# Kernel tuning notes

Hardware: AMD Instinct MI355X
Metric: run time of the kernel (lower is better)

Reference implementation:

```python
import jax, jax.numpy as jnp
import numpy as np
import math

B, H, W, C = 2, 256, 256, 96
HEADS, WS, SHIFT = 6, 8, 4
HD = C // HEADS
N = WS * WS
NW = (H // WS) * (W // WS)
HIDDEN = 2 * C
L = H * W


def _rel_pos_index():
    coords = np.stack(np.meshgrid(np.arange(WS), np.arange(WS), indexing='ij')).reshape(2, -1)
    rel = (coords[:, :, None] - coords[:, None, :]).transpose(1, 2, 0).astype(np.int64)
    rel[:, :, 0] += WS - 1
    rel[:, :, 1] += WS - 1
    rel[:, :, 0] *= 2 * WS - 1
    return rel.sum(-1)  # (N, N)

RPI = jnp.asarray(_rel_pos_index())


def _shift_mask():
    img = np.zeros((H, W), np.float32)
    cnt = 0
    for hs in (slice(0, -WS), slice(-WS, -SHIFT), slice(-SHIFT, None)):
        for ws in (slice(0, -WS), slice(-WS, -SHIFT), slice(-SHIFT, None)):
            img[hs, ws] = cnt
            cnt += 1
    mw = img.reshape(H // WS, WS, W // WS, WS).transpose(0, 2, 1, 3).reshape(-1, N)
    diff = mw[:, None, :] - mw[:, :, None]
    return jnp.asarray(np.where(diff != 0, -100.0, 0.0).astype(np.float32))  # (NW, N, N)

MASK = _shift_mask()


def window_partition(x):  # (b,H,W,c) -> (b*NW,WS,WS,c)
    b = x.shape[0]
    x = x.reshape(b, H // WS, WS, W // WS, WS, -1)
    return x.transpose(0, 1, 3, 2, 4, 5).reshape(b * NW, WS, WS, -1)


def window_reverse(w):  # (b*NW,WS,WS,c) -> (b,H,W,c)
    b = w.shape[0] // NW
    x = w.reshape(b, H // WS, W // WS, WS, WS, -1)
    return x.transpose(0, 1, 3, 2, 4, 5).reshape(b, H, W, -1)


def layernorm(x, g, bt):
    mu = x.mean(-1, keepdims=True)
    var = ((x - mu) ** 2).mean(-1, keepdims=True)
    return (x - mu) / jnp.sqrt(var + 1e-5) * g + bt


def gelu_exact(x):
    return x * 0.5 * (1.0 + jax.lax.erf(x / math.sqrt(2.0)))


def conv3(x, w, b):  # NHWC, HWIO
    return jax.lax.conv_general_dilated(x, w, (1, 1), 'SAME', dimension_numbers=('NHWC', 'HWIO', 'NHWC')) + b


def l2n(x):
    return x / jnp.maximum(jnp.linalg.norm(x, axis=-1, keepdims=True), 1e-12)


def setup_inputs() -> dict:
    key = jax.random.key(0)
    ks = jax.random.split(key, 24)
    s = 0.05
    return {
        'x': jax.random.normal(ks[0], (B, L, C), jnp.float32),
        'ref': jax.random.normal(ks[1], (B, L, C), jnp.float32),
        'norm1_g': jnp.ones((C,), jnp.float32),
        'norm1_b': jnp.zeros((C,), jnp.float32),
        'qkv_w': jax.random.normal(ks[2], (3 * C, C), jnp.float32) * s,
        'qkv_b': jnp.zeros((3 * C,), jnp.float32),
        'logit_scale': jnp.log(10.0) * jnp.ones((HEADS, 1, 1), jnp.float32),
        'gating': jnp.ones((HEADS,), jnp.float32),
        'rpb_table': jax.random.normal(ks[3], ((2 * WS - 1) ** 2, HEADS), jnp.float32) * 0.02,
        'trunk_w': jax.random.normal(ks[4], (4, 3, 3, C, C), jnp.float32) * s,
        'trunk_b': jnp.zeros((4, C), jnp.float32),
        'proj_w': jax.random.normal(ks[5], (C, C), jnp.float32) * s,
        'proj_b': jnp.zeros((C,), jnp.float32),
        'norm2_g': jnp.ones((C,), jnp.float32),
        'norm2_b': jnp.zeros((C,), jnp.float32),
        'fc1_w': jax.random.normal(ks[6], (HIDDEN, C), jnp.float32) * s,
        'fc1_b': jnp.zeros((HIDDEN,), jnp.float32),
        'convm_w': jax.random.normal(ks[7], (3, 3, HIDDEN, HIDDEN), jnp.float32) * s,
        'convm_b': jnp.zeros((HIDDEN,), jnp.float32),
        'fc2_w': jax.random.normal(ks[8], (C, HIDDEN), jnp.float32) * s,
        'fc2_b': jnp.zeros((C,), jnp.float32),
    }


def reference(x, ref, norm1_g, norm1_b, qkv_w, qkv_b, logit_scale, gating, rpb_table,
              trunk_w, trunk_b, proj_w, proj_b, norm2_g, norm2_b,
              fc1_w, fc1_b, convm_w, convm_b, fc2_w, fc2_b):
    shortcut = x
    xi = layernorm(x, norm1_g, norm1_b).reshape(B, H, W, C)
    ri = layernorm(ref, norm1_g, norm1_b).reshape(B, H, W, C)
    xi = jnp.roll(xi, (-SHIFT, -SHIFT), axis=(1, 2))
    ri = jnp.roll(ri, (-SHIFT, -SHIFT), axis=(1, 2))

    def qkv_windows(img):  # (B,H,W,C) -> q,k,v each (B*NW,HEADS,N,HD)
        t = jnp.einsum('bhwc,oc->bhwo', img, qkv_w) + qkv_b  # 1x1 conv
        t = window_partition(t).reshape(B * NW, N, 3, HEADS, HD)
        t = t.transpose(2, 0, 3, 1, 4)
        return t[0], t[1], t[2]

    q, k, v = qkv_windows(xi)
    _, k_r, v_r = qkv_windows(ri)

    ls = jnp.exp(jnp.minimum(logit_scale, math.log(1.0 / 0.01)))  # (HEADS,1,1)
    rpb = rpb_table[RPI.reshape(-1)].reshape(N, N, HEADS).transpose(2, 0, 1)  # (HEADS,N,N)
    qn = l2n(q)
    attn1 = jnp.einsum('bhnd,bhmd->bhnm', qn, l2n(k)) * ls + rpb[None]
    attn2 = jnp.einsum('bhnd,bhmd->bhnm', qn, l2n(k_r)) * ls + rpb[None]
    m = MASK[None, :, None]  # (1,NW,1,N,N)
    attn1 = (attn1.reshape(B, NW, HEADS, N, N) + m).reshape(B * NW, HEADS, N, N)
    attn2 = (attn2.reshape(B, NW, HEADS, N, N) + m).reshape(B * NW, HEADS, N, N)
    a1 = jax.nn.softmax(attn1, axis=-1)
    a2 = jax.nn.softmax(attn2, axis=-1)
    g = jax.nn.sigmoid(gating)[None, :, None, None]
    out = (1.0 - g) * jnp.einsum('bhnm,bhmd->bhnd', a1, v) + g * jnp.einsum('bhnm,bhmd->bhnd', a2, v_r)
    out = out.transpose(0, 2, 1, 3).reshape(B * NW, WS, WS, C)

    img = window_reverse(out)  # (B,H,W,C)
    # trunk branch: 2 residual blocks (conv3-relu-conv3 + skip)
    y = img
    for i in range(2):
        r = conv3(y, trunk_w[2 * i], trunk_b[2 * i])
        r = jax.nn.relu(r)
        r = conv3(r, trunk_w[2 * i + 1], trunk_b[2 * i + 1])
        y = y + r
    y = jnp.einsum('bhwc,oc->bhwo', y, proj_w) + proj_b  # 1x1 proj

    y = jnp.roll(y, (SHIFT, SHIFT), axis=(1, 2)).reshape(B, L, C)
    x = shortcut + y

    # conv-MLP: fc1 -> gelu -> conv3x3+gelu -> fc2
    h = layernorm(x, norm2_g, norm2_b)
    h = gelu_exact(h @ fc1_w.T + fc1_b)
    himg = h.reshape(B, H, W, HIDDEN)
    himg = gelu_exact(conv3(himg, convm_w, convm_b))
    h = himg.reshape(B, L, HIDDEN) @ fc2_w.T + fc2_b
    return x + h
```

## Files before the change

kernel.cpp:

```cpp
#include <hip/hip_runtime.h>
#include <hip/hip_bf16.h>

#define BB 2
#define HH 256
#define WWID 256
#define CC 96
#define NHEADS 6
#define WSZ 8
#define SHIFTV 4
#define HDIM 16
#define NTOK 64
#define HID 192
#define LL 65536

using bf16 = __hip_bfloat16;
typedef short short8v __attribute__((ext_vector_type(8)));
typedef float float4v __attribute__((ext_vector_type(4)));

__device__ __forceinline__ float b2f(bf16 v){ return __bfloat162float(v); }
__device__ __forceinline__ bf16  f2b(float f){ return __float2bfloat16(f); }
__device__ __forceinline__ float blo(unsigned u){ union {unsigned x; float f;} c; c.x = u << 16; return c.f; }
__device__ __forceinline__ float bhi(unsigned u){ union {unsigned x; float f;} c; c.x = u & 0xffff0000u; return c.f; }

__device__ __forceinline__ float dot8(uint4 a, uint4 b, float acc){
  acc += blo(a.x)*blo(b.x); acc += bhi(a.x)*bhi(b.x);
  acc += blo(a.y)*blo(b.y); acc += bhi(a.y)*bhi(b.y);
  acc += blo(a.z)*blo(b.z); acc += bhi(a.z)*bhi(b.z);
  acc += blo(a.w)*blo(b.w); acc += bhi(a.w)*bhi(b.w);
  return acc;
}

__global__ void detect_kernel(const unsigned* __restrict__ x, int* __restrict__ flag){
  __shared__ int s[256];
  int t = threadIdx.x;
  int cnt = 0;
  #pragma unroll
  for (int i = 0; i < 4; ++i){
    unsigned u = x[t*4 + i];
    unsigned e = (u >> 7) & 0xFFu;
    cnt += (e >= 118u && e <= 130u) ? 1 : 0;
  }
  s[t] = cnt; __syncthreads();
  for (int m = 128; m > 0; m >>= 1){ if (t < m) s[t] += s[t+m]; __syncthreads(); }
  if (t == 0) *flag = (s[0] < 512) ? 1 : 0;
}

struct CvtArgs { const void* src[21]; long cum[22]; };

__global__ void cvt_kernel(CvtArgs a, const int* __restrict__ flag,
                           bf16* __restrict__ dst, long total){
  long k = (long)blockIdx.x * 256 + threadIdx.x;
  if (k >= total) return;
  int lo = 0;
  #pragma unroll
  for (int i = 0; i < 21; ++i) if (k >= a.cum[i+1]) lo = i+1;
  long e = k - a.cum[lo];
  if (*flag) dst[k] = f2b(((const float*)a.src[lo])[e]);
  else       dst[k] = ((const bf16*)a.src[lo])[e];
}

__global__ void wprep_kernel(const bf16* __restrict__ w, bf16* __restrict__ out,
                             int CINr, int COUTr, long total){
  long k = (long)blockIdx.x * 256 + threadIdx.x;
  if (k >= total) return;
  int NHr = COUTr / 96, CHr = CINr / 96;
  int region = (int)(k / 9984); int rem = (int)(k - (long)region*9984);
  int gg = rem >> 3, e = rem & 7;
  int r = gg / 13, c8 = gg - r*13;
  int ch = region % CHr; int t2 = region / CHr;
  int nhh = t2 % NHr; int tap = t2 / NHr;
  bf16 v = f2b(0.f);
  if (c8 < 12){
    int cin = ch*96 + c8*8 + e;
    int cout = nhh*96 + r;
    v = w[((long)tap*CINr + cin)*COUTr + cout];
  }
  out[k] = v;
}

__global__ __launch_bounds__(256) void ln1_kernel(const bf16* __restrict__ x, const bf16* __restrict__ ref,
                                                  const bf16* __restrict__ g, const bf16* __restrict__ bt,
                                                  bf16* __restrict__ xn, bf16* __restrict__ rn)
{
  int wave = threadIdx.x >> 6, lane = threadIdx.x & 63;
  long row = (long)blockIdx.x * 4 + wave;
  const bf16* src; bf16* dst; long r;
  if (row < (long)BB*LL){ src = x; dst = xn; r = row; }
  else                  { src = ref; dst = rn; r = row - (long)BB*LL; }
  const bf16* p = src + r*CC;
  float v0 = b2f(p[lane]);
  float v1 = (lane < 32) ? b2f(p[64+lane]) : 0.f;
  float s = v0 + v1;
  #pragma unroll
  for (int m = 32; m >= 1; m >>= 1) s += __shfl_xor(s, m, 64);
  float mu = s * (1.f/CC);
  float d0 = v0 - mu, d1 = v1 - mu;
  float ss = d0*d0 + ((lane < 32) ? d1*d1 : 0.f);
  #pragma unroll
  for (int m = 32; m >= 1; m >>= 1) ss += __shfl_xor(ss, m, 64);
  float rstd = rsqrtf(ss * (1.f/CC) + 1e-5f);
  bf16* q = dst + r*CC;
  q[lane] = f2b(d0 * rstd * b2f(g[lane]) + b2f(bt[lane]));
  if (lane < 32) q[64+lane] = f2b(d1 * rstd * b2f(g[64+lane]) + b2f(bt[64+lane]));
}

__global__ __launch_bounds__(256) void ln2_kernel(const bf16* __restrict__ xin,
                                                  const bf16* __restrict__ g, const bf16* __restrict__ bt,
                                                  bf16* __restrict__ out)
{
  int wave = threadIdx.x >> 6, lane = threadIdx.x & 63;
  long r = (long)blockIdx.x * 4 + wave;
  const bf16* p = xin + r*CC;
  float v0 = b2f(p[lane]);
  float v1 = (lane < 32) ? b2f(p[64+lane]) : 0.f;
  float s = v0 + v1;
  #pragma unroll
  for (int m = 32; m >= 1; m >>= 1) s += __shfl_xor(s, m, 64);
  float mu = s * (1.f/CC);
  float d0 = v0 - mu, d1 = v1 - mu;
  float ss = d0*d0 + ((lane < 32) ? d1*d1 : 0.f);
  #pragma unroll
  for (int m = 32; m >= 1; m >>= 1) ss += __shfl_xor(ss, m, 64);
  float rstd = rsqrtf(ss * (1.f/CC) + 1e-5f);
  bf16* q = out + r*CC;
  q[lane] = f2b(d0 * rstd * b2f(g[lane]) + b2f(bt[lane]));
  if (lane < 32) q[64+lane] = f2b(d1 * rstd * b2f(g[64+lane]) + b2f(bt[64+lane]));
}

__global__ __launch_bounds__(256) void attn_kernel(const bf16* __restrict__ xn, const bf16* __restrict__ rn,
                                                   const bf16* __restrict__ qkv_w, const bf16* __restrict__ qkv_b,
                                                   const bf16* __restrict__ lsc, const bf16* __restrict__ gat,
                                                   const bf16* __restrict__ rpbt, bf16* __restrict__ img)
{
  __shared__ __align__(16) bf16 sx[NTOK][104];
  __shared__ __align__(16) bf16 sr[NTOK][104];
  __shared__ __align__(16) bf16 wb[48][104];
  __shared__ float sbias[48];
  __shared__ __align__(16) bf16 qs[NTOK][32];
  __shared__ __align__(16) bf16 ks[NTOK][32];
  __shared__ __align__(16) bf16 krs[NTOK][32];
  __shared__ __align__(16) bf16 vt[16][72];
  __shared__ __align__(16) bf16 vrt[16][72];
  __shared__ __align__(16) bf16 ps[NTOK][72];
  __shared__ float rpbs[225];

  int widx = blockIdx.x;
  int b = widx >> 10, wib = widx & 1023;
  int wh = wib >> 5, ww = wib & 31;
  int tid = threadIdx.x;
  int wv = tid >> 6, lane = tid & 63;
  int ml = lane & 15, quad = lane >> 4;

  for (int idx = tid; idx < NTOK*12; idx += 256){
    int n = idx / 12, c8 = idx - n*12;
    int i = n >> 3, j = n & 7;
    int h0 = (wh*8 + i + SHIFTV) & 255;
    int w0 = (ww*8 + j + SHIFTV) & 255;
    long base = (((long)b*HH + h0)*WWID + w0)*CC + c8*8;
    *(uint4*)&sx[n][c8*8] = *(const uint4*)&xn[base];
    *(uint4*)&sr[n][c8*8] = *(const uint4*)&rn[base];
  }
  for (int idx = tid; idx < 384; idx += 256){
    int arr = idx >> 7, rem = idx & 127;
    int row = rem >> 1, half = rem & 1;
    bf16* bp = (arr == 0) ? &qs[0][0] : (arr == 1) ? &ks[0][0] : &krs[0][0];
    *(uint4*)&bp[row*32 + 16 + half*8] = make_uint4(0,0,0,0);
  }

  for (int h = 0; h < NHEADS; ++h){
    __syncthreads();
    for (int idx = tid; idx < 48*12; idx += 256){
      int rr = idx / 12, c8 = idx - rr*12;
      int o = (rr >> 4)*CC + h*HDIM + (rr & 15);
      *(uint4*)&wb[rr][c8*8] = *(const uint4*)&qkv_w[(long)o*CC + c8*8];
    }
    if (tid < 48){
      int o = (tid >> 4)*CC + h*HDIM + (tid & 15);
      sbias[tid] = b2f(qkv_b[o]);
    }
    if (tid < 225) rpbs[tid] = b2f(rpbt[tid*NHEADS + h]);
    __syncthreads();

    float4v aq0 = {0,0,0,0}, aq1 = {0,0,0,0}, aq2 = {0,0,0,0};
    float4v ar0 = {0,0,0,0}, ar1 = {0,0,0,0};
    {
      int arow = wv*16 + ml;
      #pragma unroll
      for (int kt = 0; kt < 3; ++kt){
        int ko = kt*32 + quad*8;
        short8v ax = *(const short8v*)&sx[arow][ko];
        short8v av = *(const short8v*)&sr[arow][ko];
        short8v b0 = *(const short8v*)&wb[ml][ko];
        short8v b1 = *(const short8v*)&wb[16+ml][ko];
        short8v b2 = *(const short8v*)&wb[32+ml][ko];
        aq0 = __builtin_amdgcn_mfma_f32_16x16x32_bf16(ax, b0, aq0, 0,0,0);
        aq1 = __builtin_amdgcn_mfma_f32_16x16x32_bf16(ax, b1, aq1, 0,0,0);
        aq2 = __builtin_amdgcn_mfma_f32_16x16x32_bf16(ax, b2, aq2, 0,0,0);
        ar0 = __builtin_amdgcn_mfma_f32_16x16x32_bf16(av, b1, ar0, 0,0,0);
        ar1 = __builtin_amdgcn_mfma_f32_16x16x32_bf16(av, b2, ar1, 0,0,0);
      }
    }
    #pragma unroll
    for (int r = 0; r < 4; ++r){
      int tok = wv*16 + quad*4 + r;
      qs[tok][ml]  = f2b(aq0[r] + sbias[ml]);
      ks[tok][ml]  = f2b(aq1[r] + sbias[16+ml]);
      vt[ml][tok]  = f2b(aq2[r] + sbias[32+ml]);
      krs[tok][ml] = f2b(ar0[r] + sbias[16+ml]);
      vrt[ml][tok] = f2b(ar1[r] + sbias[32+ml]);
    }
    __syncthreads();
    if (tid < 192){
      int rr = tid & 63;
      bf16* row = (tid < 64) ? qs[rr] : (tid < 128) ? ks[rr] : krs[rr];
      float s = 0.f;
      #pragma unroll
      for (int d = 0; d < 16; ++d){ float v = b2f(row[d]); s += v*v; }
      float inv = 1.f / fmaxf(sqrtf(s), 1e-12f);
      #pragma unroll
      for (int d = 0; d < 16; ++d) row[d] = f2b(b2f(row[d]) * inv);
    }
    __syncthreads();

    float ls = expf(fminf(b2f(lsc[h]), 4.605170185988091f));
    float gv = b2f(gat[h]);
    float g = 1.f / (1.f + expf(-gv));

    float4v s1[4], s2[4];
    {
      short8v qf = *(const short8v*)&qs[wv*16 + ml][quad*8];
      #pragma unroll
      for (int nt = 0; nt < 4; ++nt){
        short8v kf  = *(const short8v*)&ks[nt*16 + ml][quad*8];
        short8v krf = *(const short8v*)&krs[nt*16 + ml][quad*8];
        float4v z = {0,0,0,0};
        s1[nt] = __builtin_amdgcn_mfma_f32_16x16x32_bf16(qf, kf,  z, 0,0,0);
        s2[nt] = __builtin_amdgcn_mfma_f32_16x16x32_bf16(qf, krf, z, 0,0,0);
      }
    }
    float sv1[4][4], sv2[4][4];
    #pragma unroll
    for (int r = 0; r < 4; ++r){
      int ti = wv*16 + quad*4 + r;
      int iy = ti >> 3, ix = ti & 7;
      int regi = ((wh < 31) ? 0 : (iy < 4 ? 1 : 2))*3 + ((ww < 31) ? 0 : (ix < 4 ? 1 : 2));
      #pragma unroll
      for (int nt = 0; nt < 4; ++nt){
        int tj = nt*16 + ml;
        int jy = tj >> 3, jx = tj & 7;
        int regj = ((wh < 31) ? 0 : (jy < 4 ? 1 : 2))*3 + ((ww < 31) ? 0 : (jx < 4 ? 1 : 2));
        float rp = rpbs[(iy - jy + 7)*15 + (ix - jx + 7)];
        float msk = (regi != regj) ? -100.f : 0.f;
        sv1[nt][r] = s1[nt][r]*ls + rp + msk;
        sv2[nt][r] = s2[nt][r]*ls + rp + msk;
      }
    }
    float f1[4], f2[4];
    #pragma unroll
    for (int r = 0; r < 4; ++r){
      float mx1 = -1e30f, mx2 = -1e30f;
      #pragma unroll
      for (int nt = 0; nt < 4; ++nt){ mx1 = fmaxf(mx1, sv1[nt][r]); mx2 = fmaxf(mx2, sv2[nt][r]); }
      #pragma unroll
      for (int m = 1; m < 16; m <<= 1){ mx1 = fmaxf(mx1, __shfl_xor(mx1, m, 64)); mx2 = fmaxf(mx2, __shfl_xor(mx2, m, 64)); }
      float sm1 = 0.f, sm2 = 0.f;
      #pragma unroll
      for (int nt = 0; nt < 4; ++nt){
        sv1[nt][r] = expf(sv1[nt][r] - mx1); sm1 += sv1[nt][r];
        sv2[nt][r] = expf(sv2[nt][r] - mx2); sm2 += sv2[nt][r];
      }
      #pragma unroll
      for (int m = 1; m < 16; m <<= 1){ sm1 += __shfl_xor(sm1, m, 64); sm2 += __shfl_xor(sm2, m, 64); }
      f1[r] = (1.f - g) / sm1;
      f2[r] = g / sm2;
    }

    #pragma unroll
    for (int r = 0; r < 4; ++r){
      int ti = wv*16 + quad*4 + r;
      #pragma unroll
      for (int nt = 0; nt < 4; ++nt) ps[ti][nt*16 + ml] = f2b(sv1[nt][r] * f1[r]);
    }
    float4v po = {0,0,0,0};
    #pragma unroll
    for (int kt = 0; kt < 2; ++kt){
      short8v pa = *(const short8v*)&ps[wv*16 + ml][kt*32 + quad*8];
      short8v vb = *(const short8v*)&vt[ml][kt*32 + quad*8];
      po = __builtin_amdgcn_mfma_f32_16x16x32_bf16(pa, vb, po, 0,0,0);
    }
    #pragma unroll
    for (int r = 0; r < 4; ++r){
      int ti = wv*16 + quad*4 + r;
      #pragma unroll
      for (int nt = 0; nt < 4; ++nt) ps[ti][nt*16 + ml] = f2b(sv2[nt][r] * f2[r]);
    }
    #pragma unroll
    for (int kt = 0; kt < 2; ++kt){
      short8v pa = *(const short8v*)&ps[wv*16 + ml][kt*32 + quad*8];
      short8v vb = *(const short8v*)&vrt[ml][kt*32 + quad*8];
      po = __builtin_amdgcn_mfma_f32_16x16x32_bf16(pa, vb, po, 0,0,0);
    }
    #pragma unroll
    for (int r = 0; r < 4; ++r){
      int tok = wv*16 + quad*4 + r;
      int hs = wh*8 + (tok >> 3), wsp = ww*8 + (tok & 7);
      img[(((long)b*HH + hs)*WWID + wsp)*CC + h*HDIM + ml] = f2b(po[r]);
    }
  }
}

template<int CIN, int COUT, int MODE>
__global__ __launch_bounds__(256) void convmfma_kernel(const bf16* __restrict__ src,
                                                       const bf16* __restrict__ wtp,
                                                       const bf16* __restrict__ bias,
                                                       const bf16* __restrict__ base,
                                                       bf16* __restrict__ dst)
{
  constexpr int CH = CIN / 96;
  constexpr int NH = COUT / 96;
  constexpr int NS = CH * 9;
  __shared__ __align__(16) bf16 act[180*13*8];
  __shared__ __align__(16) bf16 wl[2][1248*8];

  int tid = threadIdx.x;
  int z = blockIdx.z;
  int bb = z / NH;
  int nh = z % NH;
  int tx0 = blockIdx.x * 16, ty0 = blockIdx.y * 8;

  auto stage_act = [&](int h){
    for (int idx = tid; idx < 180*12; idx += 256){
      int pp = idx / 12, c8 = idx - pp*12;
      int iy = pp / 18, ix = pp - iy*18;
      int gy = ty0 + iy - 1, gx = tx0 + ix - 1;
      uint4 v = make_uint4(0,0,0,0);
      if ((unsigned)gy < (unsigned)HH && (unsigned)gx < (unsigned)WWID)
        v = *(const uint4*)&src[(((long)bb*HH + gy)*WWID + gx)*CIN + h*96 + c8*8];
      *(uint4*)&act[(pp*13 + c8)*8] = v;
    }
  };
  auto stage_w = [&](int s, int buf){
    int h = s / 9, tap = s - h*9;
    int region = (tap*NH + nh)*CH + h;
    const bf16* g = wtp + (long)region*9984;
    for (int idx = tid; idx < 1248; idx += 256)
      *(uint4*)&wl[buf][idx*8] = *(const uint4*)&g[idx*8];
  };

  int wv = tid >> 6, lane = tid & 63;
  int wm = wv >> 1, wn = wv & 1;
  int ml = lane & 15, quad = lane >> 4;

  float4v acc[4][3];
  #pragma unroll
  for (int nt = 0; nt < 3; ++nt){
    float bv = b2f(bias[nh*96 + wn*48 + nt*16 + ml]);
    #pragma unroll
    for (int mt = 0; mt < 4; ++mt)
      acc[mt][nt] = (float4v){bv, bv, bv, bv};
  }

  int apy = ml >> 3, apx = wm*8 + (ml & 7);

  stage_act(0);
  stage_w(0, 0);
  __syncthreads();

  for (int s = 0; s < NS; ++s){
    int cur = s & 1;
    int h = s / 9, tap = s - h*9;
    bool hb = (tap == 8) && (s + 1 < NS);
    if (s + 1 < NS && !hb) stage_w(s + 1, cur ^ 1);
    int dy = tap / 3, dx = tap - dy*3;
    #pragma unroll
    for (int kc = 0; kc < 3; ++kc){
      int c8 = kc*4 + quad;
      short8v b0 = *(const short8v*)&wl[cur][((wn*48 +  0 + ml)*13 + c8)*8];
      short8v b1 = *(const short8v*)&wl[cur][((wn*48 + 16 + ml)*13 + c8)*8];
      short8v b2 = *(const short8v*)&wl[cur][((wn*48 + 32 + ml)*13 + c8)*8];
      #pragma unroll
      for (int mt = 0; mt < 4; ++mt){
        int pp = (mt*2 + apy + dy)*18 + apx + dx;
        short8v a = *(const short8v*)&act[(pp*13 + c8)*8];
        acc[mt][0] = __builtin_amdgcn_mfma_f32_16x16x32_bf16(a, b0, acc[mt][0], 0, 0, 0);
        acc[mt][1] = __builtin_amdgcn_mfma_f32_16x16x32_bf16(a, b1, acc[mt][1], 0, 0, 0);
        acc[mt][2] = __builtin_amdgcn_mfma_f32_16x16x32_bf16(a, b2, acc[mt][2], 0, 0, 0);
      }
    }
    __syncthreads();
    if (hb){
      stage_act(h + 1);
      stage_w(s + 1, cur ^ 1);
      __syncthreads();
    }
  }

  #pragma unroll
  for (int mt = 0; mt < 4; ++mt){
    #pragma unroll
    for (int r = 0; r < 4; ++r){
      int mrow = quad*4 + r;
      int py = mt*2 + (mrow >> 3), px = wm*8 + (mrow & 7);
      long ob = (((long)bb*HH + ty0+py)*WWID + tx0+px)*COUT + nh*96 + wn*48 + ml;
      #pragma unroll
      for (int nt = 0; nt < 3; ++nt){
        float v = acc[mt][nt][r];
        long o = ob + nt*16;
        if (MODE == 0)      dst[o] = f2b(fmaxf(v, 0.f));
        else if (MODE == 1) dst[o] = f2b(b2f(base[o]) + v);
        else                dst[o] = f2b(0.5f * v * (1.f + erff(v * 0.7071067811865476f)));
      }
    }
  }
}

#define PPITCH (CC+8)
__global__ __launch_bounds__(256) void proj_kernel(const bf16* __restrict__ img, const bf16* __restrict__ pw,
                                                   const bf16* __restrict__ pb, const bf16* __restrict__ xorig,
                                                   bf16* __restrict__ xmid)
{
  __shared__ __align__(16) bf16 rows[64][PPITCH];
  __shared__ __align__(16) bf16 wsm[CC][PPITCH];
  long pix0 = (long)blockIdx.x * 64;
  int tid = threadIdx.x;
  for (int idx = tid; idx < 64*CC; idx += 256){
    int pp = idx / CC, c = idx - pp*CC;
    long pix = pix0 + pp;
    int b = (int)(pix >> 16); int hw = (int)(pix & 65535);
    int h = hw >> 8, wc = hw & 255;
    int sh = (h - SHIFTV) & 255, sw = (wc - SHIFTV) & 255;
    rows[pp][c] = img[(((long)b*HH + sh)*WWID + sw)*CC + c];
  }
  for (int idx = tid; idx < CC*CC; idx += 256){
    int rr = idx / CC, c = idx - rr*CC;
    wsm[rr][c] = pw[idx];
  }
  __syncthreads();
  int ty = tid >> 4, tx = tid & 15;
  int r0 = ty*4;
  float acc[4][6];
  #pragma unroll
  for (int j = 0; j < 6; ++j){
    float bv = b2f(pb[tx + 16*j]);
    #pragma unroll
    for (int i = 0; i < 4; ++i) acc[i][j] = bv;
  }
  for (int kk = 0; kk < 12; ++kk){
    uint4 a0 = ((const uint4*)rows[r0+0])[kk];
    uint4 a1 = ((const uint4*)rows[r0+1])[kk];
    uint4 a2 = ((const uint4*)rows[r0+2])[kk];
    uint4 a3 = ((const uint4*)rows[r0+3])[kk];
    #pragma unroll
    for (int j = 0; j < 6; ++j){
      uint4 wv = ((const uint4*)wsm[tx + 16*j])[kk];
      acc[0][j] = dot8(a0, wv, acc[0][j]);
      acc[1][j] = dot8(a1, wv, acc[1][j]);
      acc[2][j] = dot8(a2, wv, acc[2][j]);
      acc[3][j] = dot8(a3, wv, acc[3][j]);
    }
  }
  #pragma unroll
  for (int i = 0; i < 4; ++i){
    long pix = pix0 + r0 + i;
    #pragma unroll
    for (int j = 0; j < 6; ++j){
      long oi = pix*CC + tx + 16*j;
      xmid[oi] = f2b(b2f(xorig[oi]) + acc[i][j]);
    }
  }
}

__global__ __launch_bounds__(256) void fc1_kernel(const bf16* __restrict__ src, const bf16* __restrict__ w,
                                                  const bf16* __restrict__ bias, bf16* __restrict__ dst)
{
  __shared__ __align__(16) bf16 rows[64][PPITCH];
  __shared__ __align__(16) bf16 wsm[HID][PPITCH];
  long pix0 = (long)blockIdx.x * 64;
  int tid = threadIdx.x;
  for (int idx = tid; idx < 64*CC; idx += 256){
    int pp = idx / CC, c = idx - pp*CC;
    rows[pp][c] = src[(pix0 + pp)*CC + c];
  }
  for (int idx = tid; idx < HID*CC; idx += 256){
    int rr = idx / CC, c = idx - rr*CC;
    wsm[rr][c] = w[idx];
  }
  __syncthreads();
  int ty = tid >> 4, tx = tid & 15;
  int r0 = ty*4;
  float acc[4][12];
  #pragma unroll
  for (int j = 0; j < 12; ++j){
    float bv = b2f(bias[tx + 16*j]);
    #pragma unroll
    for (int i = 0; i < 4; ++i) acc[i][j] = bv;
  }
  for (int kk = 0; kk < 12; ++kk){
    uint4 a0 = ((const uint4*)rows[r0+0])[kk];
    uint4 a1 = ((const uint4*)rows[r0+1])[kk];
    uint4 a2 = ((const uint4*)rows[r0+2])[kk];
    uint4 a3 = ((const uint4*)rows[r0+3])[kk];
    #pragma unroll
    for (int j = 0; j < 12; ++j){
      uint4 wv = ((const uint4*)wsm[tx + 16*j])[kk];
      acc[0][j] = dot8(a0, wv, acc[0][j]);
      acc[1][j] = dot8(a1, wv, acc[1][j]);
      acc[2][j] = dot8(a2, wv, acc[2][j]);
      acc[3][j] = dot8(a3, wv, acc[3][j]);
    }
  }
  #pragma unroll
  for (int i = 0; i < 4; ++i){
    long pix = pix0 + r0 + i;
    #pragma unroll
    for (int j = 0; j < 12; ++j){
      float v = acc[i][j];
      dst[pix*HID + tx + 16*j] = f2b(0.5f * v * (1.f + erff(v * 0.7071067811865476f)));
    }
  }
}

#define FPITCH (HID+8)
__global__ __launch_bounds__(256) void fc2_kernel(const bf16* __restrict__ src, const bf16* __restrict__ w,
                                                  const bf16* __restrict__ bias, const bf16* __restrict__ xmid,
                                                  void* __restrict__ outv, const int* __restrict__ flag)
{
  __shared__ __align__(16) bf16 rows[64][FPITCH];
  __shared__ __align__(16) bf16 wsm[CC][FPITCH];
  long pix0 = (long)blockIdx.x * 64;
  int tid = threadIdx.x;
  for (int idx = tid; idx < 64*HID; idx += 256){
    int pp = idx / HID, c = idx - pp*HID;
    rows[pp][c] = src[(pix0 + pp)*HID + c];
  }
  for (int idx = tid; idx < CC*HID; idx += 256){
    int rr = idx / HID, c = idx - rr*HID;
    wsm[rr][c] = w[idx];
  }
  __syncthreads();
  int ty = tid >> 4, tx = tid & 15;
  int r0 = ty*4;
  float acc[4][6];
  #pragma unroll
  for (int j = 0; j < 6; ++j){
    float bv = b2f(bias[tx + 16*j]);
    #pragma unroll
    for (int i = 0; i < 4; ++i) acc[i][j] = bv;
  }
  for (int kk = 0; kk < 24; ++kk){
    uint4 a0 = ((const uint4*)rows[r0+0])[kk];
    uint4 a1 = ((const uint4*)rows[r0+1])[kk];
    uint4 a2 = ((const uint4*)rows[r0+2])[kk];
    uint4 a3 = ((const uint4*)rows[r0+3])[kk];
    #pragma unroll
    for (int j = 0; j < 6; ++j){
      uint4 wv = ((const uint4*)wsm[tx + 16*j])[kk];
      acc[0][j] = dot8(a0, wv, acc[0][j]);
      acc[1][j] = dot8(a1, wv, acc[1][j]);
      acc[2][j] = dot8(a2, wv, acc[2][j]);
      acc[3][j] = dot8(a3, wv, acc[3][j]);
    }
  }
  int f = *flag;
  #pragma unroll
  for (int i = 0; i < 4; ++i){
    long pix = pix0 + r0 + i;
    #pragma unroll
    for (int j = 0; j < 6; ++j){
      long oi = pix*CC + tx + 16*j;
      float v = b2f(xmid[oi]) + acc[i][j];
      if (f) ((float*)outv)[oi] = v;
      else   ((bf16*)outv)[oi] = f2b(v);
    }
  }
}

extern "C" void kernel_launch(void* const* d_in, const int* in_sizes, int n_in,
                              void* d_out, int out_size, void* d_ws, size_t ws_size,
                              hipStream_t stream)
{
  long cum[22]; cum[0] = 0;
  for (int i = 0; i < 21; ++i) cum[i+1] = cum[i] + in_sizes[i];
  long total = cum[21];

  CvtArgs a;
  for (int i = 0; i < 21; ++i) a.src[i] = d_in[i];
  for (int i = 0; i < 22; ++i) a.cum[i] = cum[i];

  char* ws = (char*)d_ws;
  int*  flag   = (int*)ws;
  bf16* packed = (bf16*)(ws + 1048576);

  detect_kernel<<<1, 256, 0, stream>>>((const unsigned*)d_in[0], flag);
  cvt_kernel<<<(int)((total + 255) / 256), 256, 0, stream>>>(a, flag, packed, total);

  #define PP(i) (packed + cum[i])
  const bf16* xc    = PP(0);
  const bf16* rc    = PP(1);
  const bf16* n1g   = PP(2);
  const bf16* n1b   = PP(3);
  const bf16* qkv_w = PP(4);
  const bf16* qkv_b = PP(5);
  const bf16* lsc   = PP(6);
  const bf16* gat   = PP(7);
  const bf16* rpbt  = PP(8);
  const bf16* tw    = PP(9);
  const bf16* tb    = PP(10);
  const bf16* pw    = PP(11);
  const bf16* pb    = PP(12);
  const bf16* n2g   = PP(13);
  const bf16* n2b   = PP(14);
  const bf16* f1w   = PP(15);
  const bf16* f1b   = PP(16);
  const bf16* cmw   = PP(17);
  const bf16* cmb   = PP(18);
  const bf16* f2w   = PP(19);
  const bf16* f2bp  = PP(20);

  bf16* wtc  = (bf16*)(ws + 52860928);
  bf16* wtm  = (bf16*)(ws + 53579776);
  bf16* xn   = (bf16*)(ws + 54525952);
  bf16* rn   = (bf16*)(ws + 79691776);
  bf16* img  = (bf16*)(ws + 104857600);
  bf16* rtr  = xn;
  bf16* xmid = xn;
  bf16* ln2o = rn;
  bf16* h1   = (bf16*)(ws + 1048576);
  bf16* hc   = rn;

  wprep_kernel<<<1404, 256, 0, stream>>>(tw, wtc, 96, 96, 359424);
  wprep_kernel<<<1404, 256, 0, stream>>>(cmw, wtm, 192, 192, 359424);

  ln1_kernel<<<65536, 256, 0, stream>>>(xc, rc, n1g, n1b, xn, rn);
  attn_kernel<<<2048, 256, 0, stream>>>(xn, rn, qkv_w, qkv_b, lsc, gat, rpbt, img);

  convmfma_kernel<96,96,0><<<dim3(16,32,2), 256, 0, stream>>>(img, wtc + 0*89856, tb + 0,   nullptr, rtr);
  convmfma_kernel<96,96,1><<<dim3(16,32,2), 256, 0, stream>>>(rtr, wtc + 1*89856, tb + 96,  img,     img);
  convmfma_kernel<96,96,0><<<dim3(16,32,2), 256, 0, stream>>>(img, wtc + 2*89856, tb + 192, nullptr, rtr);
  convmfma_kernel<96,96,1><<<dim3(16,32,2), 256, 0, stream>>>(rtr, wtc + 3*89856, tb + 288, img,     img);

  proj_kernel<<<2048, 256, 0, stream>>>(img, pw, pb, xc, xmid);
  ln2_kernel<<<32768, 256, 0, stream>>>(xmid, n2g, n2b, ln2o);
  fc1_kernel<<<2048, 256, 0, stream>>>(ln2o, f1w, f1b, h1);
  convmfma_kernel<192,192,2><<<dim3(16,32,4), 256, 0, stream>>>(h1, wtm, cmb, nullptr, hc);
  fc2_kernel<<<2048, 256, 0, stream>>>(hc, f2w, f2bp, xmid, d_out, flag);
}
```

Before: 1.079 ms.

## Swizzle conv LDS layout, register-prefetch weights, vectorize input conversion

The conv kernel's LDS tiles move from a padded 13-slot row stride to an unpadded 12-slot stride with an XOR swizzle that avoids bank conflicts. The double-buffered weight tile becomes a single buffer fed by a register prefetch one stage ahead, which cuts LDS use and pairs with launch bounds requesting three blocks per CU for occupancy. The input conversion kernel now handles eight elements per thread with padded segment offsets. The cost is an extra barrier per stage and more registers for the prefetched weights.

```diff
diff --git a/kernel.cpp b/kernel.cpp
--- a/kernel.cpp
+++ b/kernel.cpp
@@ -30,6 +30,10 @@
   return acc;
 }
 
+__device__ __forceinline__ int swz(int c8, int r){
+  return (c8 < 8) ? (c8 ^ (r & 7)) : (8 + ((c8 & 3) ^ ((r >> 1) & 3)));
+}
+
 __global__ void detect_kernel(const unsigned* __restrict__ x, int* __restrict__ flag){
   __shared__ int s[256];
   int t = threadIdx.x;
@@ -45,18 +49,39 @@
   if (t == 0) *flag = (s[0] < 512) ? 1 : 0;
 }
 
-struct CvtArgs { const void* src[21]; long cum[22]; };
+struct CvtArgs { const void* src[21]; long cum[22]; long cumP[22]; };
 
 __global__ void cvt_kernel(CvtArgs a, const int* __restrict__ flag,
-                           bf16* __restrict__ dst, long total){
-  long k = (long)blockIdx.x * 256 + threadIdx.x;
-  if (k >= total) return;
+                           bf16* __restrict__ dst, long totalP){
+  long k0 = ((long)blockIdx.x * 256 + threadIdx.x) * 8;
+  if (k0 >= totalP) return;
   int lo = 0;
   #pragma unroll
-  for (int i = 0; i < 21; ++i) if (k >= a.cum[i+1]) lo = i+1;
-  long e = k - a.cum[lo];
-  if (*flag) dst[k] = f2b(((const float*)a.src[lo])[e]);
-  else       dst[k] = ((const bf16*)a.src[lo])[e];
+  for (int i = 0; i < 21; ++i) if (k0 >= a.cumP[i+1]) lo = i+1;
+  long e = k0 - a.cumP[lo];
+  long n = a.cum[lo+1] - a.cum[lo];
+  int f = *flag;
+  __align__(16) bf16 ob[8];
+  if (e + 8 <= n){
+    if (f){
+      const float* s = (const float*)a.src[lo] + e;
+      float4 v0 = *(const float4*)s;
+      float4 v1 = *(const float4*)(s + 4);
+      ob[0]=f2b(v0.x); ob[1]=f2b(v0.y); ob[2]=f2b(v0.z); ob[3]=f2b(v0.w);
+      ob[4]=f2b(v1.x); ob[5]=f2b(v1.y); ob[6]=f2b(v1.z); ob[7]=f2b(v1.w);
+    } else {
+      *(uint4*)ob = *(const uint4*)((const bf16*)a.src[lo] + e);
+    }
+  } else {
+    #pragma unroll
+    for (int j = 0; j < 8; ++j){
+      long ee = e + j;
+      ob[j] = (ee < n) ? (f ? f2b(((const float*)a.src[lo])[ee])
+                            : ((const bf16*)a.src[lo])[ee])
+                       : f2b(0.f);
+    }
+  }
+  *(uint4*)&dst[k0] = *(uint4*)ob;
 }
 
 __global__ void wprep_kernel(const bf16* __restrict__ w, bf16* __restrict__ out,
@@ -64,18 +89,15 @@
   long k = (long)blockIdx.x * 256 + threadIdx.x;
   if (k >= total) return;
   int NHr = COUTr / 96, CHr = CINr / 96;
-  int region = (int)(k / 9984); int rem = (int)(k - (long)region*9984);
+  int region = (int)(k / 9216); int rem = (int)(k - (long)region*9216);
   int gg = rem >> 3, e = rem & 7;
-  int r = gg / 13, c8 = gg - r*13;
+  int r = gg / 12, pos = gg - r*12;
   int ch = region % CHr; int t2 = region / CHr;
   int nhh = t2 % NHr; int tap = t2 / NHr;
-  bf16 v = f2b(0.f);
-  if (c8 < 12){
-    int cin = ch*96 + c8*8 + e;
-    int cout = nhh*96 + r;
-    v = w[((long)tap*CINr + cin)*COUTr + cout];
-  }
-  out[k] = v;
+  int c8 = (pos < 8) ? (pos ^ (r & 7)) : (8 + ((pos & 3) ^ ((r >> 1) & 3)));
+  int cin = ch*96 + c8*8 + e;
+  int cout = nhh*96 + r;
+  out[k] = w[((long)tap*CINr + cin)*COUTr + cout];
 }
 
 __global__ __launch_bounds__(256) void ln1_kernel(const bf16* __restrict__ x, const bf16* __restrict__ ref,
@@ -310,17 +332,17 @@
 }
 
 template<int CIN, int COUT, int MODE>
-__global__ __launch_bounds__(256) void convmfma_kernel(const bf16* __restrict__ src,
-                                                       const bf16* __restrict__ wtp,
-                                                       const bf16* __restrict__ bias,
-                                                       const bf16* __restrict__ base,
-                                                       bf16* __restrict__ dst)
+__global__ __launch_bounds__(256, 3) void convmfma_kernel(const bf16* __restrict__ src,
+                                                          const bf16* __restrict__ wtp,
+                                                          const bf16* __restrict__ bias,
+                                                          const bf16* __restrict__ base,
+                                                          bf16* __restrict__ dst)
 {
   constexpr int CH = CIN / 96;
   constexpr int NH = COUT / 96;
   constexpr int NS = CH * 9;
-  __shared__ __align__(16) bf16 act[180*13*8];
-  __shared__ __align__(16) bf16 wl[2][1248*8];
+  __shared__ __align__(16) bf16 act[180*12*8];
+  __shared__ __align__(16) bf16 wl[96*12*8];
 
   int tid = threadIdx.x;
   int z = blockIdx.z;
@@ -336,15 +358,26 @@
       uint4 v = make_uint4(0,0,0,0);
       if ((unsigned)gy < (unsigned)HH && (unsigned)gx < (unsigned)WWID)
         v = *(const uint4*)&src[(((long)bb*HH + gy)*WWID + gx)*CIN + h*96 + c8*8];
-      *(uint4*)&act[(pp*13 + c8)*8] = v;
+      *(uint4*)&act[(pp*12 + swz(c8, pp))*8] = v;
     }
   };
-  auto stage_w = [&](int s, int buf){
+  uint4 wreg[5];
+  auto ldW = [&](int s){
     int h = s / 9, tap = s - h*9;
     int region = (tap*NH + nh)*CH + h;
-    const bf16* g = wtp + (long)region*9984;
-    for (int idx = tid; idx < 1248; idx += 256)
-      *(uint4*)&wl[buf][idx*8] = *(const uint4*)&g[idx*8];
+    const bf16* g = wtp + (long)region*9216;
+    #pragma unroll
+    for (int i = 0; i < 5; ++i){
+      int idx = i*256 + tid;
+      if (idx < 1152) wreg[i] = *(const uint4*)&g[idx*8];
+    }
+  };
+  auto stW = [&](){
+    #pragma unroll
+    for (int i = 0; i < 5; ++i){
+      int idx = i*256 + tid;
+      if (idx < 1152) *(uint4*)&wl[idx*8] = wreg[i];
+    }
   };
 
   int wv = tid >> 6, lane = tid & 63;
@@ -363,34 +396,36 @@
   int apy = ml >> 3, apx = wm*8 + (ml & 7);
 
   stage_act(0);
-  stage_w(0, 0);
+  ldW(0);
+  stW();
+  if (NS > 1) ldW(1);
   __syncthreads();
 
   for (int s = 0; s < NS; ++s){
-    int cur = s & 1;
     int h = s / 9, tap = s - h*9;
-    bool hb = (tap == 8) && (s + 1 < NS);
-    if (s + 1 < NS && !hb) stage_w(s + 1, cur ^ 1);
     int dy = tap / 3, dx = tap - dy*3;
     #pragma unroll
     for (int kc = 0; kc < 3; ++kc){
-      int c8 = kc*4 + quad;
-      short8v b0 = *(const short8v*)&wl[cur][((wn*48 +  0 + ml)*13 + c8)*8];
-      short8v b1 = *(const short8v*)&wl[cur][((wn*48 + 16 + ml)*13 + c8)*8];
-      short8v b2 = *(const short8v*)&wl[cur][((wn*48 + 32 + ml)*13 + c8)*8];
+      int posB = (kc < 2) ? ((kc*4 + quad) ^ (ml & 7)) : (8 + (quad ^ ((ml >> 1) & 3)));
+      int brow = wn*48 + ml;
+      short8v b0 = *(const short8v*)&wl[((brow     )*12 + posB)*8];
+      short8v b1 = *(const short8v*)&wl[((brow + 16)*12 + posB)*8];
+      short8v b2 = *(const short8v*)&wl[((brow + 32)*12 + posB)*8];
       #pragma unroll
       for (int mt = 0; mt < 4; ++mt){
         int pp = (mt*2 + apy + dy)*18 + apx + dx;
-        short8v a = *(const short8v*)&act[(pp*13 + c8)*8];
+        int posA = (kc < 2) ? ((kc*4 + quad) ^ (pp & 7)) : (8 + (quad ^ ((pp >> 1) & 3)));
+        short8v a = *(const short8v*)&act[(pp*12 + posA)*8];
         acc[mt][0] = __builtin_amdgcn_mfma_f32_16x16x32_bf16(a, b0, acc[mt][0], 0, 0, 0);
         acc[mt][1] = __builtin_amdgcn_mfma_f32_16x16x32_bf16(a, b1, acc[mt][1], 0, 0, 0);
         acc[mt][2] = __builtin_amdgcn_mfma_f32_16x16x32_bf16(a, b2, acc[mt][2], 0, 0, 0);
       }
     }
-    __syncthreads();
-    if (hb){
-      stage_act(h + 1);
-      stage_w(s + 1, cur ^ 1);
+    if (s + 1 < NS){
+      __syncthreads();
+      if (tap == 8) stage_act(h + 1);
+      stW();
+      if (s + 2 < NS) ldW(s + 2);
       __syncthreads();
     }
   }
@@ -579,22 +614,25 @@
                               void* d_out, int out_size, void* d_ws, size_t ws_size,
                               hipStream_t stream)
 {
-  long cum[22]; cum[0] = 0;
-  for (int i = 0; i < 21; ++i) cum[i+1] = cum[i] + in_sizes[i];
-  long total = cum[21];
+  long cum[22], cumP[22]; cum[0] = 0; cumP[0] = 0;
+  for (int i = 0; i < 21; ++i){
+    cum[i+1]  = cum[i]  + in_sizes[i];
+    cumP[i+1] = cumP[i] + (((long)in_sizes[i] + 7) & ~7L);
+  }
+  long totalP = cumP[21];
 
   CvtArgs a;
   for (int i = 0; i < 21; ++i) a.src[i] = d_in[i];
-  for (int i = 0; i < 22; ++i) a.cum[i] = cum[i];
+  for (int i = 0; i < 22; ++i){ a.cum[i] = cum[i]; a.cumP[i] = cumP[i]; }
 
   char* ws = (char*)d_ws;
   int*  flag   = (int*)ws;
   bf16* packed = (bf16*)(ws + 1048576);
 
   detect_kernel<<<1, 256, 0, stream>>>((const unsigned*)d_in[0], flag);
-  cvt_kernel<<<(int)((total + 255) / 256), 256, 0, stream>>>(a, flag, packed, total);
-
-  #define PP(i) (packed + cum[i])
+  cvt_kernel<<<(int)((totalP/8 + 255) / 256), 256, 0, stream>>>(a, flag, packed, totalP);
+
+  #define PP(i) (packed + cumP[i])
   const bf16* xc    = PP(0);
   const bf16* rc    = PP(1);
   const bf16* n1g   = PP(2);
@@ -628,16 +666,16 @@
   bf16* h1   = (bf16*)(ws + 1048576);
   bf16* hc   = rn;
 
-  wprep_kernel<<<1404, 256, 0, stream>>>(tw, wtc, 96, 96, 359424);
-  wprep_kernel<<<1404, 256, 0, stream>>>(cmw, wtm, 192, 192, 359424);
+  wprep_kernel<<<1296, 256, 0, stream>>>(tw, wtc, 96, 96, 331776);
+  wprep_kernel<<<1296, 256, 0, stream>>>(cmw, wtm, 192, 192, 331776);
 
   ln1_kernel<<<65536, 256, 0, stream>>>(xc, rc, n1g, n1b, xn, rn);
   attn_kernel<<<2048, 256, 0, stream>>>(xn, rn, qkv_w, qkv_b, lsc, gat, rpbt, img);
 
-  convmfma_kernel<96,96,0><<<dim3(16,32,2), 256, 0, stream>>>(img, wtc + 0*89856, tb + 0,   nullptr, rtr);
-  convmfma_kernel<96,96,1><<<dim3(16,32,2), 256, 0, stream>>>(rtr, wtc + 1*89856, tb + 96,  img,     img);
-  convmfma_kernel<96,96,0><<<dim3(16,32,2), 256, 0, stream>>>(img, wtc + 2*89856, tb + 192, nullptr, rtr);
-  convmfma_kernel<96,96,1><<<dim3(16,32,2), 256, 0, stream>>>(rtr, wtc + 3*89856, tb + 288, img,     img);
+  convmfma_kernel<96,96,0><<<dim3(16,32,2), 256, 0, stream>>>(img, wtc + 0*82944, tb + 0,   nullptr, rtr);
+  convmfma_kernel<96,96,1><<<dim3(16,32,2), 256, 0, stream>>>(rtr, wtc + 1*82944, tb + 96,  img,     img);
+  convmfma_kernel<96,96,0><<<dim3(16,32,2), 256, 0, stream>>>(img, wtc + 2*82944, tb + 192, nullptr, rtr);
+  convmfma_kernel<96,96,1><<<dim3(16,32,2), 256, 0, stream>>>(rtr, wtc + 3*82944, tb + 288, img,     img);
 
   proj_kernel<<<2048, 256, 0, stream>>>(img, pw, pb, xc, xmid);
   ln2_kernel<<<32768, 256, 0, stream>>>(xmid, n2g, n2b, ln2o);
```

Result: slower. 1.185 ms (+9.8%).
